# Kernel tuning notes

Measured on AMD Instinct MI355X. Metric: run time of the kernel, lower is better.

## Reference

```python
import jax, jax.numpy as jnp
import numpy as np
import math

B, T, C = 4, 2048, 1024
N_HEADS = 16
D_HEAD = C // N_HEADS


def _rope_tables(d_head, max_seq_len):
    half = d_head // 2
    theta = 1.0 / (10000.0 ** (jnp.arange(half, dtype=jnp.float32) / half))
    pos = jnp.arange(max_seq_len, dtype=jnp.float32)
    freqs = jnp.outer(pos, theta)  # [S, half]
    cos = jnp.concatenate([jnp.cos(freqs), jnp.cos(freqs)], axis=-1)  # [S, d_head]
    sin = jnp.concatenate([jnp.sin(freqs), jnp.sin(freqs)], axis=-1)
    return cos, sin


def _rotate_half(x):
    d = x.shape[-1] // 2
    return jnp.concatenate([-x[..., d:], x[..., :d]], axis=-1)


def _apply_rope(x, cos, sin):
    # x: [B, H, T, d_head]; cos/sin: [T, d_head] broadcast over B,H
    return x * cos[None, None] + _rotate_half(x) * sin[None, None]


def setup_inputs() -> dict:
    key = jax.random.key(0)
    k1, k2, k3 = jax.random.split(key, 3)
    x = jax.random.normal(k1, (B, T, C), dtype=jnp.float32)
    W_qkv = jax.random.normal(k2, (C, 3 * C), dtype=jnp.float32) * (1.0 / math.sqrt(C))
    W_proj = jax.random.normal(k3, (C, C), dtype=jnp.float32) * (1.0 / math.sqrt(C))
    return {"x": x, "W_qkv": W_qkv, "W_proj": W_proj}


def reference(x, W_qkv, W_proj):
    b, t, c = x.shape
    qkv = x @ W_qkv  # [B, T, 3C]
    q, k, v = jnp.split(qkv, 3, axis=-1)

    def reshape(z):
        return z.reshape(b, t, N_HEADS, D_HEAD).transpose(0, 2, 1, 3)  # [B,H,T,dh]

    q, k, v = reshape(q), reshape(k), reshape(v)

    cos, sin = _rope_tables(D_HEAD, t)
    q = _apply_rope(q, cos, sin)
    k = _apply_rope(k, cos, sin)

    scale = 1.0 / math.sqrt(D_HEAD)
    att = jnp.einsum('bhqd,bhkd->bhqk', q, k) * scale  # [B,H,T,T]
    causal = jnp.tril(jnp.ones((t, t), dtype=bool))
    att = jnp.where(causal[None, None], att, -jnp.inf)
    att = jax.nn.softmax(att, axis=-1)
    out = jnp.einsum('bhqk,bhkd->bhqd', att, v)  # [B,H,T,dh]
    out = out.transpose(0, 2, 1, 3).reshape(b, t, c)
    return out @ W_proj
```

## Files before the change

kernel.cpp:

```cpp
#include <hip/hip_runtime.h>
#include <stdint.h>

#define Bz 4
#define Tz 2048
#define Cz 1024
#define NHz 16
#define DHz 64
#define Mz (Bz*Tz)

typedef unsigned short u16;
typedef __attribute__((ext_vector_type(8))) short short8;
typedef __attribute__((ext_vector_type(8))) unsigned short ushort8v;
typedef __attribute__((ext_vector_type(4))) unsigned short u16x4;
typedef __attribute__((ext_vector_type(4))) float f32x4;
typedef __attribute__((ext_vector_type(2))) unsigned int uint2v;

__device__ __forceinline__ float bf2f(u16 u){
  union { unsigned int i; float f; } v; v.i = ((unsigned int)u) << 16; return v.f;
}
__device__ __forceinline__ u16 f2bf(float f){
  union { float f; unsigned int i; } v; v.f = f;
  unsigned int r = v.i + 0x7FFFu + ((v.i >> 16) & 1u);
  return (u16)(r >> 16);
}


__global__ void k_cast_bf16(const float* __restrict__ in, u16* __restrict__ out, int n4){
  int i = blockIdx.x*256 + threadIdx.x;
  if (i >= n4) return;
  float4 v = ((const float4*)in)[i];
  u16x4 o;
  o[0] = f2bf(v.x); o[1] = f2bf(v.y); o[2] = f2bf(v.z); o[3] = f2bf(v.w);
  *(u16x4*)(out + (size_t)i*4) = o;
}

__global__ void k_transpose_cast(const float* __restrict__ W, u16* __restrict__ Wt, int K, int N){
  __shared__ float tile[32][33];
  int n0 = blockIdx.x*32, k0 = blockIdx.y*32;
  int tx = threadIdx.x, ty = threadIdx.y;
  #pragma unroll
  for (int i = 0; i < 32; i += 8)
    tile[ty+i][tx] = W[(size_t)(k0+ty+i)*N + n0 + tx];
  __syncthreads();
  #pragma unroll
  for (int i = 0; i < 32; i += 8)
    Wt[(size_t)(n0+ty+i)*K + k0 + tx] = f2bf(tile[tx][ty+i]);
}

__global__ void k_rope_tables(float* __restrict__ cosT, float* __restrict__ sinT){
  int idx = blockIdx.x*256 + threadIdx.x;
  int t = idx >> 5, i = idx & 31;
  float theta = exp2f(-(float)i * (13.287712379549449f / 32.0f));
  float ang = (float)t * theta;
  cosT[idx] = cosf(ang);
  sinT[idx] = sinf(ang);
}

#define GLDS(src, dstE) __builtin_amdgcn_global_load_lds( \
    (const __attribute__((address_space(1))) unsigned int*)(src), \
    (__attribute__((address_space(3))) unsigned int*)(lds + (dstE)), 16, 0, 0)

template<int Nn, int Kk, bool OUT_BF16, bool ROPE>
__global__ __launch_bounds__(512, 2) void k_gemm8(const u16* __restrict__ A, const u16* __restrict__ Bt,
                       void* __restrict__ Cout, u16* __restrict__ vTout,
                       const float* __restrict__ cosT, const float* __restrict__ sinT){
  extern __shared__ u16 lds[];
  constexpr int NT = Kk/64;
  constexpr int BUFE = 24576;
  const int bm = blockIdx.x, bn = blockIdx.y;
  const int tid = threadIdx.x, lane = tid & 63, w = tid >> 6;
  const int wm = w >> 2, wn = w & 3;
  const int g = lane >> 4, r = lane & 15;

  const int srow8 = lane >> 3;
  const int sslot = (lane & 7) ^ srow8;
  const u16* asrc = A  + (size_t)(bm*128 + w*16 + srow8)*Kk + sslot*8;
  const u16* bsrc = Bt + (size_t)(bn*256 + w*16 + srow8)*Kk + sslot*8;
  const int dA  = w*1024 + lane*8;
  const int dB0 = 8192 + w*1024 + lane*8;
  const int dB1 = 16384 + w*1024 + lane*8;

  int a_off[2][2][2], b_off[2][2][2];
  #pragma unroll
  for (int rq = 0; rq < 2; ++rq)
    #pragma unroll
    for (int fi = 0; fi < 2; ++fi)
      #pragma unroll
      for (int kc = 0; kc < 2; ++kc){
        int row = wm*64 + rq*32 + fi*16 + r;
        a_off[rq][fi][kc] = (row*128 + kc*64 + g*16) ^ ((r & 7) << 4);
        int rowb = wn*64 + rq*32 + fi*16 + r;
        b_off[rq][fi][kc] = 16384 + ((rowb*128 + kc*64 + g*16) ^ ((r & 7) << 4));
      }

  f32x4 acc[4][4] = {};

  {
    GLDS(asrc,                     dA);        GLDS(asrc + 8*(size_t)Kk,                     dA + 512);
    GLDS(bsrc,                     dB0);       GLDS(bsrc + 8*(size_t)Kk,                     dB0 + 512);
    GLDS(bsrc + 128*(size_t)Kk,    dB1);       GLDS(bsrc + 136*(size_t)Kk,                   dB1 + 512);
    GLDS(asrc + 64,                BUFE + dA); GLDS(asrc + 64 + 8*(size_t)Kk,                BUFE + dA + 512);
    GLDS(bsrc + 64,                BUFE + dB0);GLDS(bsrc + 64 + 8*(size_t)Kk,                BUFE + dB0 + 512);
    GLDS(bsrc + 64 + 128*(size_t)Kk, BUFE + dB1); GLDS(bsrc + 64 + 136*(size_t)Kk,           BUFE + dB1 + 512);
  }

  int bufc = 0;
  #pragma unroll 1
  for (int t = 0; t < NT; ++t){
    if (t + 1 < NT) asm volatile("s_waitcnt vmcnt(6)" ::: "memory");
    else            asm volatile("s_waitcnt vmcnt(0)" ::: "memory");
    __builtin_amdgcn_s_barrier();

    const int cbB = bufc*(BUFE*2);
    const bool pre = (t + 2 < NT);
    int bufn = bufc + 2; if (bufn >= 3) bufn -= 3;
    const int nE = bufn*BUFE;
    const size_t ko = (size_t)(t+2)*64;

    #define LD8(off) (*(const short8*)((const char*)lds + (off)))
    short8 af0k0, af0k1, af1k0, af1k1;
    short8 b0f0k0, b0f0k1, b0f1k0, b0f1k1;
    short8 b1f0k0, b1f0k1, b1f1k0, b1f1k1;

    af0k0 = LD8(cbB + a_off[0][0][0]); af0k1 = LD8(cbB + a_off[0][0][1]);
    af1k0 = LD8(cbB + a_off[0][1][0]); af1k1 = LD8(cbB + a_off[0][1][1]);
    b0f0k0 = LD8(cbB + b_off[0][0][0]); b0f0k1 = LD8(cbB + b_off[0][0][1]);
    b0f1k0 = LD8(cbB + b_off[0][1][0]); b0f1k1 = LD8(cbB + b_off[0][1][1]);
    if (pre){ GLDS(asrc + ko, nE + dA); GLDS(asrc + ko + 8*(size_t)Kk, nE + dA + 512); }
    __builtin_amdgcn_s_setprio(1);
    acc[0][0] = __builtin_amdgcn_mfma_f32_16x16x32_bf16(af0k0, b0f0k0, acc[0][0], 0,0,0);
    acc[0][0] = __builtin_amdgcn_mfma_f32_16x16x32_bf16(af0k1, b0f0k1, acc[0][0], 0,0,0);
    acc[0][1] = __builtin_amdgcn_mfma_f32_16x16x32_bf16(af0k0, b0f1k0, acc[0][1], 0,0,0);
    acc[0][1] = __builtin_amdgcn_mfma_f32_16x16x32_bf16(af0k1, b0f1k1, acc[0][1], 0,0,0);
    acc[1][0] = __builtin_amdgcn_mfma_f32_16x16x32_bf16(af1k0, b0f0k0, acc[1][0], 0,0,0);
    acc[1][0] = __builtin_amdgcn_mfma_f32_16x16x32_bf16(af1k1, b0f0k1, acc[1][0], 0,0,0);
    acc[1][1] = __builtin_amdgcn_mfma_f32_16x16x32_bf16(af1k0, b0f1k0, acc[1][1], 0,0,0);
    acc[1][1] = __builtin_amdgcn_mfma_f32_16x16x32_bf16(af1k1, b0f1k1, acc[1][1], 0,0,0);
    __builtin_amdgcn_s_setprio(0);

    b1f0k0 = LD8(cbB + b_off[1][0][0]); b1f0k1 = LD8(cbB + b_off[1][0][1]);
    b1f1k0 = LD8(cbB + b_off[1][1][0]); b1f1k1 = LD8(cbB + b_off[1][1][1]);
    if (pre){ GLDS(bsrc + ko, nE + dB0); GLDS(bsrc + ko + 8*(size_t)Kk, nE + dB0 + 512); }
    __builtin_amdgcn_s_setprio(1);
    acc[0][2] = __builtin_amdgcn_mfma_f32_16x16x32_bf16(af0k0, b1f0k0, acc[0][2], 0,0,0);
    acc[0][2] = __builtin_amdgcn_mfma_f32_16x16x32_bf16(af0k1, b1f0k1, acc[0][2], 0,0,0);
    acc[0][3] = __builtin_amdgcn_mfma_f32_16x16x32_bf16(af0k0, b1f1k0, acc[0][3], 0,0,0);
    acc[0][3] = __builtin_amdgcn_mfma_f32_16x16x32_bf16(af0k1, b1f1k1, acc[0][3], 0,0,0);
    acc[1][2] = __builtin_amdgcn_mfma_f32_16x16x32_bf16(af1k0, b1f0k0, acc[1][2], 0,0,0);
    acc[1][2] = __builtin_amdgcn_mfma_f32_16x16x32_bf16(af1k1, b1f0k1, acc[1][2], 0,0,0);
    acc[1][3] = __builtin_amdgcn_mfma_f32_16x16x32_bf16(af1k0, b1f1k0, acc[1][3], 0,0,0);
    acc[1][3] = __builtin_amdgcn_mfma_f32_16x16x32_bf16(af1k1, b1f1k1, acc[1][3], 0,0,0);
    __builtin_amdgcn_s_setprio(0);

    af0k0 = LD8(cbB + a_off[1][0][0]); af0k1 = LD8(cbB + a_off[1][0][1]);
    af1k0 = LD8(cbB + a_off[1][1][0]); af1k1 = LD8(cbB + a_off[1][1][1]);
    if (pre){ GLDS(bsrc + ko + 128*(size_t)Kk, nE + dB1); GLDS(bsrc + ko + 136*(size_t)Kk, nE + dB1 + 512); }
    __builtin_amdgcn_s_setprio(1);
    acc[2][2] = __builtin_amdgcn_mfma_f32_16x16x32_bf16(af0k0, b1f0k0, acc[2][2], 0,0,0);
    acc[2][2] = __builtin_amdgcn_mfma_f32_16x16x32_bf16(af0k1, b1f0k1, acc[2][2], 0,0,0);
    acc[2][3] = __builtin_amdgcn_mfma_f32_16x16x32_bf16(af0k0, b1f1k0, acc[2][3], 0,0,0);
    acc[2][3] = __builtin_amdgcn_mfma_f32_16x16x32_bf16(af0k1, b1f1k1, acc[2][3], 0,0,0);
    acc[3][2] = __builtin_amdgcn_mfma_f32_16x16x32_bf16(af1k0, b1f0k0, acc[3][2], 0,0,0);
    acc[3][2] = __builtin_amdgcn_mfma_f32_16x16x32_bf16(af1k1, b1f0k1, acc[3][2], 0,0,0);
    acc[3][3] = __builtin_amdgcn_mfma_f32_16x16x32_bf16(af1k0, b1f1k0, acc[3][3], 0,0,0);
    acc[3][3] = __builtin_amdgcn_mfma_f32_16x16x32_bf16(af1k1, b1f1k1, acc[3][3], 0,0,0);
    __builtin_amdgcn_s_setprio(0);

    __builtin_amdgcn_s_setprio(1);
    acc[2][0] = __builtin_amdgcn_mfma_f32_16x16x32_bf16(af0k0, b0f0k0, acc[2][0], 0,0,0);
    acc[2][0] = __builtin_amdgcn_mfma_f32_16x16x32_bf16(af0k1, b0f0k1, acc[2][0], 0,0,0);
    acc[2][1] = __builtin_amdgcn_mfma_f32_16x16x32_bf16(af0k0, b0f1k0, acc[2][1], 0,0,0);
    acc[2][1] = __builtin_amdgcn_mfma_f32_16x16x32_bf16(af0k1, b0f1k1, acc[2][1], 0,0,0);
    acc[3][0] = __builtin_amdgcn_mfma_f32_16x16x32_bf16(af1k0, b0f0k0, acc[3][0], 0,0,0);
    acc[3][0] = __builtin_amdgcn_mfma_f32_16x16x32_bf16(af1k1, b0f0k1, acc[3][0], 0,0,0);
    acc[3][1] = __builtin_amdgcn_mfma_f32_16x16x32_bf16(af1k0, b0f1k0, acc[3][1], 0,0,0);
    acc[3][1] = __builtin_amdgcn_mfma_f32_16x16x32_bf16(af1k1, b0f1k1, acc[3][1], 0,0,0);
    __builtin_amdgcn_s_setprio(0);
    #undef LD8

    ++bufc; if (bufc >= 3) bufc = 0;
  }

  const int nbase = bn*256 + wn*64;
  if (ROPE && nbase >= 2048){
    const int b = (bm*128) >> 11;
    const int h = (nbase >> 6) & 15;
    #pragma unroll
    for (int ri = 0; ri < 4; ++ri){
      const int m0 = bm*128 + wm*64 + ri*16 + 4*g;
      const int t0 = m0 & (Tz-1);
      #pragma unroll
      for (int cj = 0; cj < 4; ++cj){
        const int d = cj*16 + r;
        u16x4 o;
        #pragma unroll
        for (int jj = 0; jj < 4; ++jj) o[jj] = f2bf(acc[ri][cj][jj]);
        *(u16x4*)(vTout + ((size_t)((b*16 + h)*64 + d))*2048 + t0) = o;
      }
    }
  } else if (ROPE){
    const float qs = (nbase < 1024) ? 0.18033688011112042f : 1.0f;
    #pragma unroll
    for (int ri = 0; ri < 4; ++ri)
      #pragma unroll
      for (int jj = 0; jj < 4; ++jj){
        const int m = bm*128 + wm*64 + ri*16 + 4*g + jj;
        const int t = m & (Tz-1);
        #pragma unroll
        for (int cj = 0; cj < 2; ++cj){
          const int ch = cj*16 + r;
          float cv = cosT[t*32 + ch];
          float sv = sinT[t*32 + ch];
          float lo = acc[ri][cj][jj], hi = acc[ri][cj+2][jj];
          ((u16*)Cout)[(size_t)m*Nn + nbase + ch]      = f2bf((lo*cv - hi*sv)*qs);
          ((u16*)Cout)[(size_t)m*Nn + nbase + ch + 32] = f2bf((hi*cv + lo*sv)*qs);
        }
      }
  } else {
    #pragma unroll
    for (int ri = 0; ri < 4; ++ri)
      #pragma unroll
      for (int cj = 0; cj < 4; ++cj)
        #pragma unroll
        for (int jj = 0; jj < 4; ++jj){
          const size_t m = bm*128 + wm*64 + ri*16 + 4*g + jj;
          const size_t n = (size_t)nbase + cj*16 + r;
          if (OUT_BF16) ((u16*)Cout)[m*Nn + n] = f2bf(acc[ri][cj][jj]);
          else          ((float*)Cout)[m*Nn + n] = acc[ri][cj][jj];
        }
  }
}

__global__ __launch_bounds__(512) void k_attn2(const u16* __restrict__ qkv,
                                               const u16* __restrict__ vT,
                                               u16* __restrict__ att){
  __shared__ u16 K_lds[2*4096];
  __shared__ u16 V_lds[2*4096];
  __shared__ u16 P_lds[8*16*72];

  const int bh = blockIdx.y;
  const int b = bh >> 4, h = bh & 15;
  const int tid = threadIdx.x;
  const int w = tid >> 6;
  const int lane = tid & 63;
  const int g = lane >> 4;
  const int ql = lane & 15;
  u16* Pw = P_lds + w*16*72;

  const int srow  = lane >> 3;
  const int sslot = (lane & 7) ^ srow;
  const u16* ksrc = qkv + ((size_t)(b*Tz + 8*w + srow))*3072 + 1024 + h*64 + sslot*8;
  const u16* vsrc = vT  + ((size_t)bh*64 + 8*w + srow)*2048 + sslot*8;
  u16* kdst = K_lds + w*512 + lane*8;
  u16* vdst = V_lds + w*512 + lane*8;

  int fofs[4][2];
  #pragma unroll
  for (int t = 0; t < 4; ++t){
    int row = 16*t + ql;
    fofs[t][0] = (row*128 + 16*g)      ^ ((row & 7) << 4);
    fofs[t][1] = (row*128 + 64 + 16*g) ^ ((row & 7) << 4);
  }

  #pragma unroll 1
  for (int half = 0; half < 2; ++half){
    const int qt = (half == 0) ? blockIdx.x : (15 - blockIdx.x);
    const int qr0w = qt*128 + w*16;
    const int nt = 2*qt + 2;

    const u16* qsrc = qkv + (size_t)(b*Tz + qr0w + ql)*3072 + h*64;
    short8 qf0 = *(const short8*)(qsrc + g*8);
    short8 qf1 = *(const short8*)(qsrc + 32 + g*8);

    float l_run = 0.0f;
    f32x4 acc[4] = {{0,0,0,0},{0,0,0,0},{0,0,0,0},{0,0,0,0}};

    __builtin_amdgcn_global_load_lds(
      (const __attribute__((address_space(1))) unsigned int*)(ksrc),
      (__attribute__((address_space(3))) unsigned int*)(kdst), 16, 0, 0);
    __builtin_amdgcn_global_load_lds(
      (const __attribute__((address_space(1))) unsigned int*)(vsrc),
      (__attribute__((address_space(3))) unsigned int*)(vdst), 16, 0, 0);
    __syncthreads();

    #pragma unroll 2
    for (int kt = 0; kt < nt; ++kt){
      const int buf = kt & 1;
      if (kt + 1 < nt){
        __builtin_amdgcn_global_load_lds(
          (const __attribute__((address_space(1))) unsigned int*)(ksrc + (size_t)(kt+1)*64*3072),
          (__attribute__((address_space(3))) unsigned int*)(kdst + (buf^1)*4096), 16, 0, 0);
        __builtin_amdgcn_global_load_lds(
          (const __attribute__((address_space(1))) unsigned int*)(vsrc + (kt+1)*64),
          (__attribute__((address_space(3))) unsigned int*)(vdst + (buf^1)*4096), 16, 0, 0);
      }
      const char* Kb = (const char*)(K_lds + buf*4096);
      const char* Vb = (const char*)(V_lds + buf*4096);
      const int kv0 = kt*64;

      f32x4 st[4];
      __builtin_amdgcn_s_setprio(1);
      #pragma unroll
      for (int t = 0; t < 4; ++t){
        short8 kf0 = *(const short8*)(Kb + fofs[t][0]);
        short8 kf1 = *(const short8*)(Kb + fofs[t][1]);
        f32x4 z = {0,0,0,0};
        z = __builtin_amdgcn_mfma_f32_16x16x32_bf16(kf0, qf0, z, 0, 0, 0);
        z = __builtin_amdgcn_mfma_f32_16x16x32_bf16(kf1, qf1, z, 0, 0, 0);
        st[t] = z;
      }
      __builtin_amdgcn_s_setprio(0);

      if (kv0 + 63 > qr0w){
        const int qg = qr0w + ql;
        #pragma unroll
        for (int t = 0; t < 4; ++t)
          #pragma unroll
          for (int j = 0; j < 4; ++j)
            if (kv0 + 16*t + 4*g + j > qg) st[t][j] = -1e30f;
      }

      #pragma unroll
      for (int t = 0; t < 4; ++t){
        float p0 = exp2f(st[t][0]);
        float p1 = exp2f(st[t][1]);
        float p2 = exp2f(st[t][2]);
        float p3 = exp2f(st[t][3]);
        l_run += (p0+p1)+(p2+p3);
        unsigned int lov, hiv;
        asm("v_cvt_pk_bf16_f32 %0, %1, %2" : "=v"(lov) : "v"(p0), "v"(p1));
        asm("v_cvt_pk_bf16_f32 %0, %1, %2" : "=v"(hiv) : "v"(p2), "v"(p3));
        uint2v pv; pv[0] = lov; pv[1] = hiv;
        *(uint2v*)((char*)Pw + ql*144 + (16*t + 4*g)*2) = pv;
      }

      short8 pf0 = *(const short8*)((char*)Pw + ql*144 + 16*g);
      short8 pf1 = *(const short8*)((char*)Pw + ql*144 + 64 + 16*g);
      __builtin_amdgcn_s_setprio(1);
      #pragma unroll
      for (int dt = 0; dt < 4; ++dt){
        short8 vf0 = *(const short8*)(Vb + fofs[dt][0]);
        short8 vf1 = *(const short8*)(Vb + fofs[dt][1]);
        acc[dt] = __builtin_amdgcn_mfma_f32_16x16x32_bf16(pf0, vf0, acc[dt], 0, 0, 0);
        acc[dt] = __builtin_amdgcn_mfma_f32_16x16x32_bf16(pf1, vf1, acc[dt], 0, 0, 0);
      }
      __builtin_amdgcn_s_setprio(0);
      __syncthreads();
    }

    l_run += __shfl_xor(l_run, 16);
    l_run += __shfl_xor(l_run, 32);
    float linv = 1.0f / l_run;
    float l0 = __shfl(linv, 4*g+0);
    float l1 = __shfl(linv, 4*g+1);
    float l2 = __shfl(linv, 4*g+2);
    float l3 = __shfl(linv, 4*g+3);
    #pragma unroll
    for (int dt = 0; dt < 4; ++dt){
      float lj[4] = {l0, l1, l2, l3};
      #pragma unroll
      for (int j = 0; j < 4; ++j)
        att[(size_t)(b*Tz + qr0w + 4*g + j)*Cz + h*64 + dt*16 + ql] = f2bf(acc[dt][j]*lj[j]);
    }
  }
}


extern "C" void kernel_launch(void* const* d_in, const int* in_sizes, int n_in,
                              void* d_out, int out_size, void* d_ws, size_t ws_size,
                              hipStream_t stream){
  const float* x     = (const float*)d_in[0];
  const float* Wqkv  = (const float*)d_in[1];
  const float* Wproj = (const float*)d_in[2];
  float* out = (float*)d_out;
  char* ws = (char*)d_ws;

  u16*  xb   = (u16*)(ws);
  u16*  wqt  = (u16*)(ws + 16777216);
  u16*  wpt  = (u16*)(ws + 23068672);
  u16*  qkv  = (u16*)(ws + 25165824);
  u16*  vTr  = (u16*)(ws + 75497472);
  float* cosT = (float*)(ws + 92274688);
  float* sinT = (float*)(ws + 92536832);

  hipFuncSetAttribute(reinterpret_cast<const void*>(k_gemm8<3072,1024,true,true>),
                      hipFuncAttributeMaxDynamicSharedMemorySize, 147456);
  hipFuncSetAttribute(reinterpret_cast<const void*>(k_gemm8<1024,1024,false,false>),
                      hipFuncAttributeMaxDynamicSharedMemorySize, 147456);

  k_cast_bf16<<<Mz*Cz/4/256, 256, 0, stream>>>(x, xb, Mz*Cz/4);
  k_transpose_cast<<<dim3(3072/32, 1024/32), dim3(32,8), 0, stream>>>(Wqkv, wqt, 1024, 3072);
  k_transpose_cast<<<dim3(1024/32, 1024/32), dim3(32,8), 0, stream>>>(Wproj, wpt, 1024, 1024);
  k_rope_tables<<<Tz*32/256, 256, 0, stream>>>(cosT, sinT);

  k_gemm8<3072, 1024, true, true><<<dim3(Mz/128, 3072/256), 512, 147456, stream>>>(
      xb, wqt, qkv, vTr, cosT, sinT);
  k_attn2<<<dim3(8, Bz*NHz), 512, 0, stream>>>(qkv, vTr, xb);
  k_gemm8<1024, 1024, false, false><<<dim3(Mz/128, 1024/256), 512, 147456, stream>>>(
      xb, wpt, out, nullptr, nullptr, nullptr);
}
```

Baseline: 177.8 us.

## Remap GEMM/attention workgroups for XCD locality and compute row sums via MFMA

GEMM kernels now use a 1D grid with a workgroup index remap so that consecutive blocks on the same XCD (blockIdx mod 8) cover contiguous tile ranges, improving L2 reuse of A/B tiles. The attention grid is transposed so heads vary fastest, which changes which blocks share an XCD. The softmax denominator is computed by an extra MFMA of P against a ones vector instead of scalar adds and cross-lane shuffles, and exp2f is replaced with raw v_exp_f32. This trades two extra MFMAs per tile for fewer VALU ops, and the row sum is now taken from the bf16-rounded P values.

```diff
diff --git a/kernel.cpp b/kernel.cpp
--- a/kernel.cpp
+++ b/kernel.cpp
@@ -67,7 +67,9 @@
   extern __shared__ u16 lds[];
   constexpr int NT = Kk/64;
   constexpr int BUFE = 24576;
-  const int bm = blockIdx.x, bn = blockIdx.y;
+  constexpr int NWG = (Mz/128)*(Nn/256);
+  const int wg = (blockIdx.x & 7)*(NWG/8) + (blockIdx.x >> 3);
+  const int bm = wg & 63, bn = wg >> 6;
   const int tid = threadIdx.x, lane = tid & 63, w = tid >> 6;
   const int wm = w >> 2, wn = w & 3;
   const int g = lane >> 4, r = lane & 15;
@@ -238,7 +240,7 @@
   __shared__ u16 V_lds[2*4096];
   __shared__ u16 P_lds[8*16*72];
 
-  const int bh = blockIdx.y;
+  const int bh = blockIdx.x;
   const int b = bh >> 4, h = bh & 15;
   const int tid = threadIdx.x;
   const int w = tid >> 6;
@@ -254,6 +256,10 @@
   u16* kdst = K_lds + w*512 + lane*8;
   u16* vdst = V_lds + w*512 + lane*8;
 
+  short8 ones;
+  #pragma unroll
+  for (int i = 0; i < 8; ++i) ones[i] = (short)0x3F80;
+
   int fofs[4][2];
   #pragma unroll
   for (int t = 0; t < 4; ++t){
@@ -264,7 +270,7 @@
 
   #pragma unroll 1
   for (int half = 0; half < 2; ++half){
-    const int qt = (half == 0) ? blockIdx.x : (15 - blockIdx.x);
+    const int qt = (half == 0) ? blockIdx.y : (15 - blockIdx.y);
     const int qr0w = qt*128 + w*16;
     const int nt = 2*qt + 2;
 
@@ -272,8 +278,8 @@
     short8 qf0 = *(const short8*)(qsrc + g*8);
     short8 qf1 = *(const short8*)(qsrc + 32 + g*8);
 
-    float l_run = 0.0f;
     f32x4 acc[4] = {{0,0,0,0},{0,0,0,0},{0,0,0,0},{0,0,0,0}};
+    f32x4 accl = {0,0,0,0};
 
     __builtin_amdgcn_global_load_lds(
       (const __attribute__((address_space(1))) unsigned int*)(ksrc),
@@ -322,11 +328,11 @@
 
       #pragma unroll
       for (int t = 0; t < 4; ++t){
-        float p0 = exp2f(st[t][0]);
-        float p1 = exp2f(st[t][1]);
-        float p2 = exp2f(st[t][2]);
-        float p3 = exp2f(st[t][3]);
-        l_run += (p0+p1)+(p2+p3);
+        float p0, p1, p2, p3;
+        asm("v_exp_f32 %0, %1" : "=v"(p0) : "v"(st[t][0]));
+        asm("v_exp_f32 %0, %1" : "=v"(p1) : "v"(st[t][1]));
+        asm("v_exp_f32 %0, %1" : "=v"(p2) : "v"(st[t][2]));
+        asm("v_exp_f32 %0, %1" : "=v"(p3) : "v"(st[t][3]));
         unsigned int lov, hiv;
         asm("v_cvt_pk_bf16_f32 %0, %1, %2" : "=v"(lov) : "v"(p0), "v"(p1));
         asm("v_cvt_pk_bf16_f32 %0, %1, %2" : "=v"(hiv) : "v"(p2), "v"(p3));
@@ -337,6 +343,8 @@
       short8 pf0 = *(const short8*)((char*)Pw + ql*144 + 16*g);
       short8 pf1 = *(const short8*)((char*)Pw + ql*144 + 64 + 16*g);
       __builtin_amdgcn_s_setprio(1);
+      accl = __builtin_amdgcn_mfma_f32_16x16x32_bf16(pf0, ones, accl, 0, 0, 0);
+      accl = __builtin_amdgcn_mfma_f32_16x16x32_bf16(pf1, ones, accl, 0, 0, 0);
       #pragma unroll
       for (int dt = 0; dt < 4; ++dt){
         short8 vf0 = *(const short8*)(Vb + fofs[dt][0]);
@@ -348,20 +356,14 @@
       __syncthreads();
     }
 
-    l_run += __shfl_xor(l_run, 16);
-    l_run += __shfl_xor(l_run, 32);
-    float linv = 1.0f / l_run;
-    float l0 = __shfl(linv, 4*g+0);
-    float l1 = __shfl(linv, 4*g+1);
-    float l2 = __shfl(linv, 4*g+2);
-    float l3 = __shfl(linv, 4*g+3);
-    #pragma unroll
-    for (int dt = 0; dt < 4; ++dt){
-      float lj[4] = {l0, l1, l2, l3};
+    float lj[4];
+    #pragma unroll
+    for (int j = 0; j < 4; ++j) lj[j] = 1.0f / accl[j];
+    #pragma unroll
+    for (int dt = 0; dt < 4; ++dt)
       #pragma unroll
       for (int j = 0; j < 4; ++j)
         att[(size_t)(b*Tz + qr0w + 4*g + j)*Cz + h*64 + dt*16 + ql] = f2bf(acc[dt][j]*lj[j]);
-    }
   }
 }
 
@@ -393,9 +395,9 @@
   k_transpose_cast<<<dim3(1024/32, 1024/32), dim3(32,8), 0, stream>>>(Wproj, wpt, 1024, 1024);
   k_rope_tables<<<Tz*32/256, 256, 0, stream>>>(cosT, sinT);
 
-  k_gemm8<3072, 1024, true, true><<<dim3(Mz/128, 3072/256), 512, 147456, stream>>>(
+  k_gemm8<3072, 1024, true, true><<<(Mz/128)*(3072/256), 512, 147456, stream>>>(
       xb, wqt, qkv, vTr, cosT, sinT);
-  k_attn2<<<dim3(8, Bz*NHz), 512, 0, stream>>>(qkv, vTr, xb);
-  k_gemm8<1024, 1024, false, false><<<dim3(Mz/128, 1024/256), 512, 147456, stream>>>(
+  k_attn2<<<dim3(Bz*NHz, 8), 512, 0, stream>>>(qkv, vTr, xb);
+  k_gemm8<1024, 1024, false, false><<<(Mz/128)*(1024/256), 512, 147456, stream>>>(
       xb, wpt, out, nullptr, nullptr, nullptr);
 }
```

After: 161.5 us. -9.1%, faster.
